# Performance work log

Hardware: AMD Instinct MI355X
Metric: run time of the kernel (lower is better)

The kernel has to match this reference:

```python
import jax, jax.numpy as jnp
import numpy as np

N_NODES = 100000
N_EDGES = 1600000
IN_F, HID_F, OUT_F = 128, 256, 64


def setup_inputs() -> dict:
    key = jax.random.key(0)
    ks = jax.random.split(key, 10)
    feats = jax.random.normal(ks[0], (N_NODES, IN_F), dtype=jnp.float32)
    edge_src = jax.random.randint(ks[1], (N_EDGES,), 0, N_NODES, dtype=jnp.int32)
    edge_dst = jax.random.randint(ks[2], (N_EDGES,), 0, N_NODES, dtype=jnp.int32)

    def glorot(k, shape):
        fan_in, fan_out = shape[1], shape[0]
        lim = np.sqrt(6.0 / (fan_in + fan_out)).astype(np.float32)
        return jax.random.uniform(k, shape, jnp.float32, -lim, lim)

    # layer 0: in -> hid, layer 1: hid -> hid, layer 2: hid -> out
    W0_self = glorot(ks[3], (HID_F, IN_F))
    W0_neigh = glorot(ks[4], (HID_F, IN_F))
    b0 = jnp.zeros((HID_F,), jnp.float32)
    W1_self = glorot(ks[5], (HID_F, HID_F))
    W1_neigh = glorot(ks[6], (HID_F, HID_F))
    b1 = jnp.zeros((HID_F,), jnp.float32)
    W2_self = glorot(ks[7], (OUT_F, HID_F))
    W2_neigh = glorot(ks[8], (OUT_F, HID_F))
    b2 = jnp.zeros((OUT_F,), jnp.float32)
    return {
        "features": feats, "edge_src": edge_src, "edge_dst": edge_dst,
        "W0_self": W0_self, "W0_neigh": W0_neigh, "b0": b0,
        "W1_self": W1_self, "W1_neigh": W1_neigh, "b1": b1,
        "W2_self": W2_self, "W2_neigh": W2_neigh, "b2": b2,
    }


def _mean_aggregate(h, src, dst, n_nodes):
    # gather source features per edge, scatter-sum to destinations, divide by in-degree
    msgs = h[src]                                            # [E, d]
    agg = jax.ops.segment_sum(msgs, dst, num_segments=n_nodes)  # [N, d]
    deg = jax.ops.segment_sum(jnp.ones_like(dst, dtype=h.dtype), dst, num_segments=n_nodes)
    deg = jnp.maximum(deg, 1.0)
    return agg / deg[:, None]


def _sage_conv(h, src, dst, W_self, W_neigh, b, act):
    h_neigh = _mean_aggregate(h, src, dst, h.shape[0])
    out = h @ W_self.T + h_neigh @ W_neigh.T + b
    return act(out) if act is not None else out


def reference(features, edge_src, edge_dst,
              W0_self, W0_neigh, b0,
              W1_self, W1_neigh, b1,
              W2_self, W2_neigh, b2):
    h = _sage_conv(features, edge_src, edge_dst, W0_self, W0_neigh, b0, jax.nn.relu)
    h = _sage_conv(h, edge_src, edge_dst, W1_self, W1_neigh, b1, jax.nn.relu)
    h = _sage_conv(h, edge_src, edge_dst, W2_self, W2_neigh, b2, None)
    return h
```

## Files before the change

### kernel.cpp

```cpp
#include <hip/hip_runtime.h>


constexpr int NN = 100000;
constexpr int NE = 1600000;

typedef short s16x8 __attribute__((ext_vector_type(8)));
typedef float f32x4 __attribute__((ext_vector_type(4)));

struct ushort4_t { unsigned short x, y, z, w; };
struct ushort2_t { unsigned short x, y; };

__device__ __forceinline__ float bf2f(unsigned short u) {
    union { unsigned int i; float f; } c; c.i = ((unsigned int)u) << 16; return c.f;
}
__device__ __forceinline__ unsigned short f2bf(float f) {
    union { float f; unsigned int i; } c; c.f = f;
    unsigned int r = (c.i + 0x7fffu + ((c.i >> 16) & 1u)) >> 16;
    return (unsigned short)r;
}

__global__ void deg_hist_kernel(const int* __restrict__ dst, int* __restrict__ degi, int n) {
    int e = blockIdx.x * blockDim.x + threadIdx.x;
    if (e < n) atomicAdd(&degi[dst[e]], 1);
}

constexpr int SCHUNK = 1024;
constexpr int NCH = (NN + SCHUNK - 1) / SCHUNK;
constexpr int NB = (NN + 255) / 256;

__global__ void chunk_sum_kernel(const int* __restrict__ degi, int* __restrict__ csum) {
    __shared__ int red[256];
    const int blk = blockIdx.x, t = threadIdx.x;
    const int base = blk * SCHUNK + t * 4;
    int s = 0;
#pragma unroll
    for (int u = 0; u < 4; ++u) { const int i = base + u; if (i < NN) s += degi[i]; }
    red[t] = s;
    __syncthreads();
    for (int o = 128; o > 0; o >>= 1) {
        if (t < o) red[t] += red[t + o];
        __syncthreads();
    }
    if (t == 0) csum[blk] = red[0];
}

__global__ void chunk_scan_kernel(const int* __restrict__ csum, int* __restrict__ coff,
                                  int* __restrict__ row_start) {
    __shared__ int sh[128];
    const int t = threadIdx.x;
    const int v0 = (t < NCH) ? csum[t] : 0;
    sh[t] = v0;
    __syncthreads();
    for (int o = 1; o < 128; o <<= 1) {
        const int v = (t >= o) ? sh[t - o] : 0;
        __syncthreads();
        sh[t] += v;
        __syncthreads();
    }
    if (t < NCH) coff[t] = sh[t] - v0;
    if (t == 0) row_start[NN] = NE;
}

__global__ void scan_write_kernel(const int* __restrict__ degi, const int* __restrict__ coff,
                                  int* __restrict__ row_start, int* __restrict__ gcur,
                                  float* __restrict__ rdeg) {
    __shared__ int sh[256];
    const int blk = blockIdx.x, t = threadIdx.x;
    const int base = blk * SCHUNK + t * 4;
    int d[4]; int s = 0;
#pragma unroll
    for (int u = 0; u < 4; ++u) { const int i = base + u; d[u] = (i < NN) ? degi[i] : 0; s += d[u]; }
    sh[t] = s;
    __syncthreads();
    for (int o = 1; o < 256; o <<= 1) {
        const int v = (t >= o) ? sh[t - o] : 0;
        __syncthreads();
        sh[t] += v;
        __syncthreads();
    }
    int run = coff[blk] + sh[t] - s;
#pragma unroll
    for (int u = 0; u < 4; ++u) {
        const int i = base + u;
        if (i < NN) {
            row_start[i] = run;
            if ((i & 255) == 0) gcur[i >> 8] = run;
            rdeg[i] = 1.0f / (float)max(d[u], 1);
            run += d[u];
        }
    }
}

constexpr int EPB_A = 4096;
__global__ __launch_bounds__(256) void bucket_scatter_kernel(
    const int* __restrict__ src, const int* __restrict__ dst,
    int* __restrict__ gcur, int2* __restrict__ ebuf) {
    __shared__ int hist[NB];
    __shared__ int base[NB];
    const int blk = blockIdx.x, t = threadIdx.x;
    int myS[16], myD[16];
#pragma unroll
    for (int u = 0; u < 16; ++u) {
        const int i = blk * EPB_A + u * 256 + t;
        if (i < NE) { myS[u] = src[i]; myD[u] = dst[i]; } else myD[u] = -1;
    }
    for (int b = t; b < NB; b += 256) hist[b] = 0;
    __syncthreads();
#pragma unroll
    for (int u = 0; u < 16; ++u)
        if (myD[u] >= 0) atomicAdd(&hist[myD[u] >> 8], 1);
    __syncthreads();
    for (int b = t; b < NB; b += 256) {
        const int c = hist[b];
        base[b] = c ? atomicAdd(&gcur[b], c) : 0;
    }
    __syncthreads();
    for (int b = t; b < NB; b += 256) hist[b] = 0;
    __syncthreads();
#pragma unroll
    for (int u = 0; u < 16; ++u)
        if (myD[u] >= 0) {
            const int bk = myD[u] >> 8;
            const int off = atomicAdd(&hist[bk], 1);
            ebuf[base[bk] + off] = make_int2(myS[u], myD[u]);
        }
}

__global__ __launch_bounds__(256) void bucket_fill_kernel(
    const int2* __restrict__ ebuf, const int* __restrict__ row_start,
    int* __restrict__ csr) {
    __shared__ int lcur[256];
    const int b = blockIdx.x, t = threadIdx.x;
    const int nbase = b << 8;
    const int nend = min(nbase + 256, NN);
    if (nbase + t < nend) lcur[t] = row_start[nbase + t];
    __syncthreads();
    const int beg = row_start[nbase];
    const int end = row_start[nend];
    for (int i = beg + t; i < end; i += 256) {
        const int2 e = ebuf[i];
        const int p = atomicAdd(&lcur[e.y & 255], 1);
        csr[p] = e.x;
    }
}

__global__ void cvt_f32_bf16(const float* __restrict__ src, unsigned short* __restrict__ dst, int nquad) {
    int i = blockIdx.x * blockDim.x + threadIdx.x;
    if (i >= nquad) return;
    const float4 v = reinterpret_cast<const float4*>(src)[i];
    ushort4_t o = { f2bf(v.x), f2bf(v.y), f2bf(v.z), f2bf(v.w) };
    reinterpret_cast<ushort4_t*>(dst)[i] = o;
}

__global__ void cvt_weights(const float* a, const float* b, const float* c,
                            const float* d, const float* e, const float* f,
                            unsigned short* __restrict__ o) {
    int i = blockIdx.x * blockDim.x + threadIdx.x;
    int q = i * 4;
    if (q >= 229376) return;
    const float* s; int off;
    if      (q <  32768) { s = a; off = 0; }
    else if (q <  65536) { s = b; off = 32768; }
    else if (q < 131072) { s = c; off = 65536; }
    else if (q < 196608) { s = d; off = 131072; }
    else if (q < 212992) { s = e; off = 196608; }
    else                 { s = f; off = 212992; }
    const float4 v = *reinterpret_cast<const float4*>(s + (q - off));
    ushort4_t ov = { f2bf(v.x), f2bf(v.y), f2bf(v.z), f2bf(v.w) };
    *reinterpret_cast<ushort4_t*>(o + q) = ov;
}

template<int D>
__global__ __launch_bounds__(256) void gather_mean_bf16(
    const unsigned short* __restrict__ rows, const int* __restrict__ row_start,
    const int* __restrict__ csr, const float* __restrict__ rdeg,
    unsigned short* __restrict__ out) {
    constexpr int VPL = D / 64;
    const int node = (int)((blockIdx.x * (unsigned)blockDim.x + threadIdx.x) >> 6);
    if (node >= NN) return;
    const int lane = threadIdx.x & 63;
    const int beg = row_start[node];
    const int end = row_start[node + 1];
    float acc[VPL];
#pragma unroll
    for (int u = 0; u < VPL; ++u) acc[u] = 0.f;

    auto accum = [&](int s) {
        const unsigned short* p = rows + (size_t)s * D + lane * VPL;
        if constexpr (VPL == 4) {
            const ushort4_t v = *reinterpret_cast<const ushort4_t*>(p);
            acc[0] += bf2f(v.x); acc[1] += bf2f(v.y); acc[2] += bf2f(v.z); acc[3] += bf2f(v.w);
        } else if constexpr (VPL == 2) {
            const ushort2_t v = *reinterpret_cast<const ushort2_t*>(p);
            acc[0] += bf2f(v.x); acc[1] += bf2f(v.y);
        } else {
            acc[0] += bf2f(*p);
        }
    };

    int e = beg;
    for (; e + 8 <= end; e += 8) {
        const int s0 = csr[e],     s1 = csr[e + 1], s2 = csr[e + 2], s3 = csr[e + 3];
        const int s4 = csr[e + 4], s5 = csr[e + 5], s6 = csr[e + 6], s7 = csr[e + 7];
        accum(s0); accum(s1); accum(s2); accum(s3);
        accum(s4); accum(s5); accum(s6); accum(s7);
    }
    for (; e + 4 <= end; e += 4) {
        const int s0 = csr[e], s1 = csr[e + 1], s2 = csr[e + 2], s3 = csr[e + 3];
        accum(s0); accum(s1); accum(s2); accum(s3);
    }
    for (; e < end; ++e) accum(csr[e]);

    const float r = rdeg[node];
    unsigned short* o = out + (size_t)node * D + lane * VPL;
    if constexpr (VPL == 4) {
        ushort4_t v = { f2bf(acc[0] * r), f2bf(acc[1] * r), f2bf(acc[2] * r), f2bf(acc[3] * r) };
        *reinterpret_cast<ushort4_t*>(o) = v;
    } else if constexpr (VPL == 2) {
        ushort2_t v = { f2bf(acc[0] * r), f2bf(acc[1] * r) };
        *reinterpret_cast<ushort2_t*>(o) = v;
    } else {
        *o = f2bf(acc[0] * r);
    }
}

template<int K1, int K2, int F, int BN, bool RELU, bool HASBIAS, bool HASADD, bool OUTBF16>
__global__ __launch_bounds__(256, 2) void mfma_gemm(
    const unsigned short* A1, const unsigned short* A2,
    const unsigned short* __restrict__ W1, const unsigned short* __restrict__ W2,
    const float* __restrict__ bias, const unsigned short* __restrict__ addC,
    void* outp) {

    constexpr int BM = 128, BK = 64;
    constexpr int KA = K1 + K2;
    constexpr int WN = BN / 2;
    constexpr int FM = 4, FN = WN / 16;
    constexpr int ABASE = 0;
    constexpr int BBASE = BM * BK * 2;
    constexpr int B_ITERS = (BN * 8) / 256;

    __shared__ __align__(16) char smem[(BM + BN) * BK * 2];

    const int tid = threadIdx.x;
    const int l = tid & 63;
    const int w = tid >> 6;
    const int wr = w >> 1, wc = w & 1;
    const int lr = l & 15, lhi = l >> 4;
    const int bm = blockIdx.x * BM;
    const int bn = blockIdx.y * BN;

    f32x4 acc[FM][FN];
#pragma unroll
    for (int i = 0; i < FM; ++i)
#pragma unroll
        for (int j = 0; j < FN; ++j) acc[i][j] = (f32x4){0.f, 0.f, 0.f, 0.f};

    int rowA[FM], rowB[FN];
#pragma unroll
    for (int fm = 0; fm < FM; ++fm) rowA[fm] = wr * 64 + fm * 16 + lr;
#pragma unroll
    for (int fn = 0; fn < FN; ++fn) rowB[fn] = wc * WN + fn * 16 + lr;

    for (int k0 = 0; k0 < KA; k0 += BK) {
        const bool inR1 = (k0 < K1);
        const unsigned short* Ap = inR1 ? A1 : A2;
        const unsigned short* Wp = inR1 ? W1 : W2;
        const int stride = inR1 ? K1 : K2;
        const int kk0 = inR1 ? k0 : (k0 - K1);

#pragma unroll
        for (int it = 0; it < 4; ++it) {
            const int s = tid + it * 256;
            const int m = s >> 3;
            const int kseg = s & 7;
            float4 v = make_float4(0.f, 0.f, 0.f, 0.f);
            const int mg = bm + m;
            if (mg < NN)
                v = *reinterpret_cast<const float4*>(Ap + (size_t)mg * stride + kk0 + kseg * 8);
            *reinterpret_cast<float4*>(smem + ABASE + m * 128 + ((kseg ^ (m & 7)) << 4)) = v;
        }
#pragma unroll
        for (int it = 0; it < B_ITERS; ++it) {
            const int s = tid + it * 256;
            const int f = s >> 3;
            const int kseg = s & 7;
            const float4 v = *reinterpret_cast<const float4*>(
                Wp + (size_t)(bn + f) * stride + kk0 + kseg * 8);
            *reinterpret_cast<float4*>(smem + BBASE + f * 128 + ((kseg ^ (f & 7)) << 4)) = v;
        }
        __syncthreads();

#pragma unroll
        for (int ksub = 0; ksub < 2; ++ksub) {
            const int kb = ksub * 4 + lhi;
            s16x8 a[FM], b[FN];
#pragma unroll
            for (int fm = 0; fm < FM; ++fm)
                a[fm] = *reinterpret_cast<const s16x8*>(
                    smem + ABASE + rowA[fm] * 128 + ((kb ^ (rowA[fm] & 7)) << 4));
#pragma unroll
            for (int fn = 0; fn < FN; ++fn)
                b[fn] = *reinterpret_cast<const s16x8*>(
                    smem + BBASE + rowB[fn] * 128 + ((kb ^ (rowB[fn] & 7)) << 4));
#pragma unroll
            for (int fm = 0; fm < FM; ++fm)
#pragma unroll
                for (int fn = 0; fn < FN; ++fn)
                    acc[fm][fn] = __builtin_amdgcn_mfma_f32_16x16x32_bf16(
                        a[fm], b[fn], acc[fm][fn], 0, 0, 0);
        }
        __syncthreads();
    }

#pragma unroll
    for (int fn = 0; fn < FN; ++fn) {
        const int col = bn + wc * WN + fn * 16 + lr;
        const float bv = HASBIAS ? bias[col] : 0.f;
#pragma unroll
        for (int fm = 0; fm < FM; ++fm) {
#pragma unroll
            for (int r = 0; r < 4; ++r) {
                const int row = bm + wr * 64 + fm * 16 + lhi * 4 + r;
                if (row >= NN) continue;
                float v = acc[fm][fn][r] + bv;
                if (HASADD) v += bf2f(addC[(size_t)row * F + col]);
                if (RELU) v = fmaxf(v, 0.f);
                if (OUTBF16)
                    ((unsigned short*)outp)[(size_t)row * F + col] = f2bf(v);
                else
                    ((float*)outp)[(size_t)row * F + col] = v;
            }
        }
    }
}

extern "C" void kernel_launch(void* const* d_in, const int* in_sizes, int n_in,
                              void* d_out, int out_size, void* d_ws, size_t ws_size,
                              hipStream_t stream) {
    const float* feats = (const float*)d_in[0];
    const int*   esrc  = (const int*)d_in[1];
    const int*   edst  = (const int*)d_in[2];
    const float* W0s = (const float*)d_in[3];
    const float* W0n = (const float*)d_in[4];
    const float* b0  = (const float*)d_in[5];
    const float* W1s = (const float*)d_in[6];
    const float* W1n = (const float*)d_in[7];
    const float* b1  = (const float*)d_in[8];
    const float* W2s = (const float*)d_in[9];
    const float* W2n = (const float*)d_in[10];
    const float* b2  = (const float*)d_in[11];
    float* out = (float*)d_out;

    char* p = (char*)d_ws;
    auto alloc = [&](size_t bytes) { char* r = p; p += (bytes + 255) & ~255ull; return r; };
    int*   degi      = (int*)alloc((size_t)NN * 4);
    int*   row_start = (int*)alloc(((size_t)NN + 1) * 4);
    int*   gcur      = (int*)alloc((size_t)NB * 4);
    int*   csr       = (int*)alloc((size_t)NE * 4);
    int2*  ebuf      = (int2*)alloc((size_t)NE * 8);
    float* rdeg      = (float*)alloc((size_t)NN * 4);
    int*   csum      = (int*)alloc((size_t)NCH * 4);
    int*   coff      = (int*)alloc((size_t)NCH * 4);
    unsigned short* wbuf = (unsigned short*)alloc((size_t)229376 * 2);
    unsigned short* fx   = (unsigned short*)alloc((size_t)NN * 128 * 2);
    unsigned short* agg  = (unsigned short*)alloc((size_t)NN * 256 * 2);
    unsigned short* h1   = (unsigned short*)alloc((size_t)NN * 256 * 2);
    unsigned short* h2   = (unsigned short*)alloc((size_t)NN * 256 * 2);
    unsigned short* z    = agg;
    unsigned short* aggz = agg + (size_t)NN * 64;

    const unsigned short* w0s = wbuf;
    const unsigned short* w0n = wbuf + 32768;
    const unsigned short* w1s = wbuf + 65536;
    const unsigned short* w1n = wbuf + 131072;
    const unsigned short* w2s = wbuf + 196608;
    const unsigned short* w2n = wbuf + 212992;

    hipMemsetAsync(degi, 0, (size_t)NN * 4, stream);
    deg_hist_kernel<<<(NE + 255) / 256, 256, 0, stream>>>(edst, degi, NE);
    chunk_sum_kernel<<<NCH, 256, 0, stream>>>(degi, csum);
    chunk_scan_kernel<<<1, 128, 0, stream>>>(csum, coff, row_start);
    scan_write_kernel<<<NCH, 256, 0, stream>>>(degi, coff, row_start, gcur, rdeg);
    bucket_scatter_kernel<<<(NE + EPB_A - 1) / EPB_A, 256, 0, stream>>>(esrc, edst, gcur, ebuf);
    bucket_fill_kernel<<<NB, 256, 0, stream>>>(ebuf, row_start, csr);

    cvt_f32_bf16<<<(NN * 128 / 4 + 255) / 256, 256, 0, stream>>>(feats, fx, NN * 128 / 4);
    cvt_weights<<<(229376 / 4 + 255) / 256, 256, 0, stream>>>(W0s, W0n, W1s, W1n, W2s, W2n, wbuf);

    const int gather_grid = (NN + 3) / 4;
    const dim3 g256((NN + 127) / 128, 2);
    const dim3 g64((NN + 127) / 128, 1);

    gather_mean_bf16<128><<<gather_grid, 256, 0, stream>>>(fx, row_start, csr, rdeg, agg);
    mfma_gemm<128, 128, 256, 128, true, true, false, true>
        <<<g256, 256, 0, stream>>>(fx, agg, w0s, w0n, b0, nullptr, h1);

    gather_mean_bf16<256><<<gather_grid, 256, 0, stream>>>(h1, row_start, csr, rdeg, agg);
    mfma_gemm<256, 256, 256, 128, true, true, false, true>
        <<<g256, 256, 0, stream>>>(h1, agg, w1s, w1n, b1, nullptr, h2);

    mfma_gemm<256, 0, 64, 64, false, false, false, true>
        <<<g64, 256, 0, stream>>>(h2, nullptr, w2n, nullptr, nullptr, nullptr, z);
    gather_mean_bf16<64><<<gather_grid, 256, 0, stream>>>(z, row_start, csr, rdeg, aggz);
    mfma_gemm<256, 0, 64, 64, false, true, true, false>
        <<<g64, 256, 0, stream>>>(h2, nullptr, w2s, nullptr, b2, aggz, out);
}
```

Baseline: 619.0 us.

## Double-buffer GEMM shared-memory tiles using direct global-to-LDS loads

Replaces the register-staged global-to-LDS copy in the MFMA GEMM with `global_load_lds` 16-byte transfers that write straight into shared memory. The XOR swizzle now moves to the global address side. It also adds a two-stage ping-pong buffer, so the next K tile is fetched while MFMAs run on the current one, and drops one barrier per iteration. Out-of-range rows are clamped to row 0 instead of zero-filled. The cost is double the shared memory per block, which may lower occupancy for wider tiles.

```diff
diff --git a/kernel.cpp b/kernel.cpp
--- a/kernel.cpp
+++ b/kernel.cpp
@@ -17,6 +17,12 @@
     union { float f; unsigned int i; } c; c.f = f;
     unsigned int r = (c.i + 0x7fffu + ((c.i >> 16) & 1u)) >> 16;
     return (unsigned short)r;
+}
+
+__device__ __forceinline__ void gl16(const void* g, void* l) {
+    __builtin_amdgcn_global_load_lds(
+        (const __attribute__((address_space(1))) unsigned int*)g,
+        (__attribute__((address_space(3))) unsigned int*)l, 16, 0, 0);
 }
 
 __global__ void deg_hist_kernel(const int* __restrict__ dst, int* __restrict__ degi, int n) {
@@ -235,11 +241,11 @@
     constexpr int KA = K1 + K2;
     constexpr int WN = BN / 2;
     constexpr int FM = 4, FN = WN / 16;
-    constexpr int ABASE = 0;
     constexpr int BBASE = BM * BK * 2;
+    constexpr int BUFSZ = (BM + BN) * BK * 2;
     constexpr int B_ITERS = (BN * 8) / 256;
 
-    __shared__ __align__(16) char smem[(BM + BN) * BK * 2];
+    __shared__ __align__(16) char smem[2][BUFSZ];
 
     const int tid = threadIdx.x;
     const int l = tid & 63;
@@ -261,35 +267,37 @@
 #pragma unroll
     for (int fn = 0; fn < FN; ++fn) rowB[fn] = wc * WN + fn * 16 + lr;
 
-    for (int k0 = 0; k0 < KA; k0 += BK) {
+    auto stage = [&](int buf, int k0) {
         const bool inR1 = (k0 < K1);
         const unsigned short* Ap = inR1 ? A1 : A2;
         const unsigned short* Wp = inR1 ? W1 : W2;
         const int stride = inR1 ? K1 : K2;
         const int kk0 = inR1 ? k0 : (k0 - K1);
-
+        char* sb = smem[buf];
 #pragma unroll
         for (int it = 0; it < 4; ++it) {
             const int s = tid + it * 256;
-            const int m = s >> 3;
-            const int kseg = s & 7;
-            float4 v = make_float4(0.f, 0.f, 0.f, 0.f);
-            const int mg = bm + m;
-            if (mg < NN)
-                v = *reinterpret_cast<const float4*>(Ap + (size_t)mg * stride + kk0 + kseg * 8);
-            *reinterpret_cast<float4*>(smem + ABASE + m * 128 + ((kseg ^ (m & 7)) << 4)) = v;
+            const int m = s >> 3, kseg = s & 7;
+            int mg = bm + m;
+            if (mg >= NN) mg = 0;
+            gl16(Ap + (size_t)mg * stride + kk0 + ((kseg ^ (m & 7)) << 3), sb + s * 16);
         }
 #pragma unroll
         for (int it = 0; it < B_ITERS; ++it) {
             const int s = tid + it * 256;
-            const int f = s >> 3;
-            const int kseg = s & 7;
-            const float4 v = *reinterpret_cast<const float4*>(
-                Wp + (size_t)(bn + f) * stride + kk0 + kseg * 8);
-            *reinterpret_cast<float4*>(smem + BBASE + f * 128 + ((kseg ^ (f & 7)) << 4)) = v;
-        }
-        __syncthreads();
-
+            const int f = s >> 3, kseg = s & 7;
+            gl16(Wp + (size_t)(bn + f) * stride + kk0 + ((kseg ^ (f & 7)) << 3),
+                 sb + BBASE + s * 16);
+        }
+    };
+
+    stage(0, 0);
+    __syncthreads();
+
+    int cur = 0;
+    for (int k0 = 0; k0 < KA; k0 += BK) {
+        if (k0 + BK < KA) stage(cur ^ 1, k0 + BK);
+        const char* sb = smem[cur];
 #pragma unroll
         for (int ksub = 0; ksub < 2; ++ksub) {
             const int kb = ksub * 4 + lhi;
@@ -297,11 +305,11 @@
 #pragma unroll
             for (int fm = 0; fm < FM; ++fm)
                 a[fm] = *reinterpret_cast<const s16x8*>(
-                    smem + ABASE + rowA[fm] * 128 + ((kb ^ (rowA[fm] & 7)) << 4));
+                    sb + rowA[fm] * 128 + ((kb ^ (rowA[fm] & 7)) << 4));
 #pragma unroll
             for (int fn = 0; fn < FN; ++fn)
                 b[fn] = *reinterpret_cast<const s16x8*>(
-                    smem + BBASE + rowB[fn] * 128 + ((kb ^ (rowB[fn] & 7)) << 4));
+                    sb + BBASE + rowB[fn] * 128 + ((kb ^ (rowB[fn] & 7)) << 4));
 #pragma unroll
             for (int fm = 0; fm < FM; ++fm)
 #pragma unroll
@@ -310,6 +318,7 @@
                         a[fm], b[fn], acc[fm][fn], 0, 0, 0);
         }
         __syncthreads();
+        cur ^= 1;
     }
 
 #pragma unroll
```

After: 629.6 us. No clear change (+1.7%).

## Build CSR via bucket counts and use sub-wavefront gathers with wider loads

Applied to the files above, without the earlier changes.

Replaces the per-node degree histogram, with its global atomics and three-kernel scan, by a block-local bucket count, a single-block bucket scan, and a bucket_build kernel. That kernel computes per-node degrees, row_start and rdeg in shared memory before filling the CSR. Separately, the gather kernels now assign sub-wavefront groups of 32 or 16 lanes per node with 16-byte loads, so more nodes are processed per wave and loads are wider. The build change removes a memset, several launches and 1.6M global atomics. The cost is an extra pass over ebuf and less lane-level parallelism per node.

```diff
diff --git a/kernel.cpp b/kernel.cpp
--- a/kernel.cpp
+++ b/kernel.cpp
@@ -5,10 +5,10 @@
 constexpr int NE = 1600000;
 
 typedef short s16x8 __attribute__((ext_vector_type(8)));
+typedef unsigned short u16x8 __attribute__((ext_vector_type(8)));
 typedef float f32x4 __attribute__((ext_vector_type(4)));
 
 struct ushort4_t { unsigned short x, y, z, w; };
-struct ushort2_t { unsigned short x, y; };
 
 __device__ __forceinline__ float bf2f(unsigned short u) {
     union { unsigned int i; float f; } c; c.i = ((unsigned int)u) << 16; return c.f;
@@ -19,79 +19,43 @@
     return (unsigned short)r;
 }
 
-__global__ void deg_hist_kernel(const int* __restrict__ dst, int* __restrict__ degi, int n) {
-    int e = blockIdx.x * blockDim.x + threadIdx.x;
-    if (e < n) atomicAdd(&degi[dst[e]], 1);
-}
-
-constexpr int SCHUNK = 1024;
-constexpr int NCH = (NN + SCHUNK - 1) / SCHUNK;
 constexpr int NB = (NN + 255) / 256;
-
-__global__ void chunk_sum_kernel(const int* __restrict__ degi, int* __restrict__ csum) {
-    __shared__ int red[256];
+constexpr int EPB_A = 4096;
+constexpr int NBLK_E = (NE + EPB_A - 1) / EPB_A;
+
+__global__ __launch_bounds__(256) void bucket_count_kernel(
+    const int* __restrict__ dst, int* __restrict__ bcnt) {
+    __shared__ int hist[NB];
     const int blk = blockIdx.x, t = threadIdx.x;
-    const int base = blk * SCHUNK + t * 4;
-    int s = 0;
-#pragma unroll
-    for (int u = 0; u < 4; ++u) { const int i = base + u; if (i < NN) s += degi[i]; }
-    red[t] = s;
-    __syncthreads();
-    for (int o = 128; o > 0; o >>= 1) {
-        if (t < o) red[t] += red[t + o];
-        __syncthreads();
-    }
-    if (t == 0) csum[blk] = red[0];
-}
-
-__global__ void chunk_scan_kernel(const int* __restrict__ csum, int* __restrict__ coff,
-                                  int* __restrict__ row_start) {
-    __shared__ int sh[128];
+    for (int b = t; b < NB; b += 256) hist[b] = 0;
+    __syncthreads();
+#pragma unroll
+    for (int u = 0; u < 16; ++u) {
+        const int i = blk * EPB_A + u * 256 + t;
+        if (i < NE) atomicAdd(&hist[dst[i] >> 8], 1);
+    }
+    __syncthreads();
+    for (int b = t; b < NB; b += 256)
+        if (hist[b]) atomicAdd(&bcnt[b], hist[b]);
+}
+
+__global__ void bucket_scan_kernel(const int* __restrict__ bcnt, int* __restrict__ bbase,
+                                   int* __restrict__ gcur, int* __restrict__ row_start) {
+    __shared__ int sh[512];
     const int t = threadIdx.x;
-    const int v0 = (t < NCH) ? csum[t] : 0;
+    const int v0 = (t < NB) ? bcnt[t] : 0;
     sh[t] = v0;
     __syncthreads();
-    for (int o = 1; o < 128; o <<= 1) {
+    for (int o = 1; o < 512; o <<= 1) {
         const int v = (t >= o) ? sh[t - o] : 0;
         __syncthreads();
         sh[t] += v;
         __syncthreads();
     }
-    if (t < NCH) coff[t] = sh[t] - v0;
-    if (t == 0) row_start[NN] = NE;
-}
-
-__global__ void scan_write_kernel(const int* __restrict__ degi, const int* __restrict__ coff,
-                                  int* __restrict__ row_start, int* __restrict__ gcur,
-                                  float* __restrict__ rdeg) {
-    __shared__ int sh[256];
-    const int blk = blockIdx.x, t = threadIdx.x;
-    const int base = blk * SCHUNK + t * 4;
-    int d[4]; int s = 0;
-#pragma unroll
-    for (int u = 0; u < 4; ++u) { const int i = base + u; d[u] = (i < NN) ? degi[i] : 0; s += d[u]; }
-    sh[t] = s;
-    __syncthreads();
-    for (int o = 1; o < 256; o <<= 1) {
-        const int v = (t >= o) ? sh[t - o] : 0;
-        __syncthreads();
-        sh[t] += v;
-        __syncthreads();
-    }
-    int run = coff[blk] + sh[t] - s;
-#pragma unroll
-    for (int u = 0; u < 4; ++u) {
-        const int i = base + u;
-        if (i < NN) {
-            row_start[i] = run;
-            if ((i & 255) == 0) gcur[i >> 8] = run;
-            rdeg[i] = 1.0f / (float)max(d[u], 1);
-            run += d[u];
-        }
-    }
-}
-
-constexpr int EPB_A = 4096;
+    if (t < NB) { const int e = sh[t] - v0; bbase[t] = e; gcur[t] = e; }
+    if (t == 0) { bbase[NB] = NE; row_start[NN] = NE; }
+}
+
 __global__ __launch_bounds__(256) void bucket_scatter_kernel(
     const int* __restrict__ src, const int* __restrict__ dst,
     int* __restrict__ gcur, int2* __restrict__ ebuf) {
@@ -126,17 +90,36 @@
         }
 }
 
-__global__ __launch_bounds__(256) void bucket_fill_kernel(
-    const int2* __restrict__ ebuf, const int* __restrict__ row_start,
-    int* __restrict__ csr) {
+__global__ __launch_bounds__(256) void bucket_build_kernel(
+    const int2* __restrict__ ebuf, const int* __restrict__ bbase,
+    int* __restrict__ row_start, float* __restrict__ rdeg, int* __restrict__ csr) {
+    __shared__ int deg[256];
+    __shared__ int sh[256];
     __shared__ int lcur[256];
     const int b = blockIdx.x, t = threadIdx.x;
-    const int nbase = b << 8;
-    const int nend = min(nbase + 256, NN);
-    if (nbase + t < nend) lcur[t] = row_start[nbase + t];
-    __syncthreads();
-    const int beg = row_start[nbase];
-    const int end = row_start[nend];
+    const int beg = bbase[b], end = bbase[b + 1];
+    deg[t] = 0;
+    __syncthreads();
+    for (int i = beg + t; i < end; i += 256)
+        atomicAdd(&deg[ebuf[i].y & 255], 1);
+    __syncthreads();
+    const int d = deg[t];
+    sh[t] = d;
+    __syncthreads();
+    for (int o = 1; o < 256; o <<= 1) {
+        const int v = (t >= o) ? sh[t - o] : 0;
+        __syncthreads();
+        sh[t] += v;
+        __syncthreads();
+    }
+    const int node = (b << 8) + t;
+    const int rs = beg + sh[t] - d;
+    if (node < NN) {
+        row_start[node] = rs;
+        rdeg[node] = 1.0f / (float)max(d, 1);
+    }
+    lcur[t] = rs;
+    __syncthreads();
     for (int i = beg + t; i < end; i += 256) {
         const int2 e = ebuf[i];
         const int p = atomicAdd(&lcur[e.y & 255], 1);
@@ -170,31 +153,34 @@
     *reinterpret_cast<ushort4_t*>(o + q) = ov;
 }
 
-template<int D>
+template<int D, int SUBW>
 __global__ __launch_bounds__(256) void gather_mean_bf16(
     const unsigned short* __restrict__ rows, const int* __restrict__ row_start,
     const int* __restrict__ csr, const float* __restrict__ rdeg,
     unsigned short* __restrict__ out) {
-    constexpr int VPL = D / 64;
-    const int node = (int)((blockIdx.x * (unsigned)blockDim.x + threadIdx.x) >> 6);
+    constexpr int BPL = 2 * D / SUBW;
+    constexpr int EPL = BPL / 2;
+    constexpr int NPB = 256 / SUBW;
+    const int sg   = threadIdx.x / SUBW;
+    const int lane = threadIdx.x % SUBW;
+    const int node = blockIdx.x * NPB + sg;
     if (node >= NN) return;
-    const int lane = threadIdx.x & 63;
     const int beg = row_start[node];
     const int end = row_start[node + 1];
-    float acc[VPL];
-#pragma unroll
-    for (int u = 0; u < VPL; ++u) acc[u] = 0.f;
+
+    float acc[EPL];
+#pragma unroll
+    for (int u = 0; u < EPL; ++u) acc[u] = 0.f;
 
     auto accum = [&](int s) {
-        const unsigned short* p = rows + (size_t)s * D + lane * VPL;
-        if constexpr (VPL == 4) {
+        const unsigned short* p = rows + (size_t)s * D + lane * EPL;
+        if constexpr (BPL == 16) {
+            const u16x8 v = *reinterpret_cast<const u16x8*>(p);
+#pragma unroll
+            for (int u = 0; u < 8; ++u) acc[u] += bf2f((unsigned short)v[u]);
+        } else {
             const ushort4_t v = *reinterpret_cast<const ushort4_t*>(p);
             acc[0] += bf2f(v.x); acc[1] += bf2f(v.y); acc[2] += bf2f(v.z); acc[3] += bf2f(v.w);
-        } else if constexpr (VPL == 2) {
-            const ushort2_t v = *reinterpret_cast<const ushort2_t*>(p);
-            acc[0] += bf2f(v.x); acc[1] += bf2f(v.y);
-        } else {
-            acc[0] += bf2f(*p);
         }
     };
 
@@ -205,22 +191,18 @@
         accum(s0); accum(s1); accum(s2); accum(s3);
         accum(s4); accum(s5); accum(s6); accum(s7);
     }
-    for (; e + 4 <= end; e += 4) {
-        const int s0 = csr[e], s1 = csr[e + 1], s2 = csr[e + 2], s3 = csr[e + 3];
-        accum(s0); accum(s1); accum(s2); accum(s3);
-    }
     for (; e < end; ++e) accum(csr[e]);
 
     const float r = rdeg[node];
-    unsigned short* o = out + (size_t)node * D + lane * VPL;
-    if constexpr (VPL == 4) {
+    unsigned short* o = out + (size_t)node * D + lane * EPL;
+    if constexpr (BPL == 16) {
+        u16x8 v;
+#pragma unroll
+        for (int u = 0; u < 8; ++u) v[u] = (unsigned short)f2bf(acc[u] * r);
+        *reinterpret_cast<u16x8*>(o) = v;
+    } else {
         ushort4_t v = { f2bf(acc[0] * r), f2bf(acc[1] * r), f2bf(acc[2] * r), f2bf(acc[3] * r) };
         *reinterpret_cast<ushort4_t*>(o) = v;
-    } else if constexpr (VPL == 2) {
-        ushort2_t v = { f2bf(acc[0] * r), f2bf(acc[1] * r) };
-        *reinterpret_cast<ushort2_t*>(o) = v;
-    } else {
-        *o = f2bf(acc[0] * r);
     }
 }
 
@@ -353,14 +335,13 @@
 
     char* p = (char*)d_ws;
     auto alloc = [&](size_t bytes) { char* r = p; p += (bytes + 255) & ~255ull; return r; };
-    int*   degi      = (int*)alloc((size_t)NN * 4);
     int*   row_start = (int*)alloc(((size_t)NN + 1) * 4);
+    int*   bcnt      = (int*)alloc((size_t)NB * 4);
+    int*   bbase     = (int*)alloc(((size_t)NB + 1) * 4);
     int*   gcur      = (int*)alloc((size_t)NB * 4);
     int*   csr       = (int*)alloc((size_t)NE * 4);
     int2*  ebuf      = (int2*)alloc((size_t)NE * 8);
     float* rdeg      = (float*)alloc((size_t)NN * 4);
-    int*   csum      = (int*)alloc((size_t)NCH * 4);
-    int*   coff      = (int*)alloc((size_t)NCH * 4);
     unsigned short* wbuf = (unsigned short*)alloc((size_t)229376 * 2);
     unsigned short* fx   = (unsigned short*)alloc((size_t)NN * 128 * 2);
     unsigned short* agg  = (unsigned short*)alloc((size_t)NN * 256 * 2);
@@ -376,32 +357,29 @@
     const unsigned short* w2s = wbuf + 196608;
     const unsigned short* w2n = wbuf + 212992;
 
-    hipMemsetAsync(degi, 0, (size_t)NN * 4, stream);
-    deg_hist_kernel<<<(NE + 255) / 256, 256, 0, stream>>>(edst, degi, NE);
-    chunk_sum_kernel<<<NCH, 256, 0, stream>>>(degi, csum);
-    chunk_scan_kernel<<<1, 128, 0, stream>>>(csum, coff, row_start);
-    scan_write_kernel<<<NCH, 256, 0, stream>>>(degi, coff, row_start, gcur, rdeg);
-    bucket_scatter_kernel<<<(NE + EPB_A - 1) / EPB_A, 256, 0, stream>>>(esrc, edst, gcur, ebuf);
-    bucket_fill_kernel<<<NB, 256, 0, stream>>>(ebuf, row_start, csr);
+    hipMemsetAsync(bcnt, 0, (size_t)NB * 4, stream);
+    bucket_count_kernel<<<NBLK_E, 256, 0, stream>>>(edst, bcnt);
+    bucket_scan_kernel<<<1, 512, 0, stream>>>(bcnt, bbase, gcur, row_start);
+    bucket_scatter_kernel<<<NBLK_E, 256, 0, stream>>>(esrc, edst, gcur, ebuf);
+    bucket_build_kernel<<<NB, 256, 0, stream>>>(ebuf, bbase, row_start, rdeg, csr);
 
     cvt_f32_bf16<<<(NN * 128 / 4 + 255) / 256, 256, 0, stream>>>(feats, fx, NN * 128 / 4);
     cvt_weights<<<(229376 / 4 + 255) / 256, 256, 0, stream>>>(W0s, W0n, W1s, W1n, W2s, W2n, wbuf);
 
-    const int gather_grid = (NN + 3) / 4;
     const dim3 g256((NN + 127) / 128, 2);
     const dim3 g64((NN + 127) / 128, 1);
 
-    gather_mean_bf16<128><<<gather_grid, 256, 0, stream>>>(fx, row_start, csr, rdeg, agg);
+    gather_mean_bf16<128, 32><<<(NN + 7) / 8, 256, 0, stream>>>(fx, row_start, csr, rdeg, agg);
     mfma_gemm<128, 128, 256, 128, true, true, false, true>
         <<<g256, 256, 0, stream>>>(fx, agg, w0s, w0n, b0, nullptr, h1);
 
-    gather_mean_bf16<256><<<gather_grid, 256, 0, stream>>>(h1, row_start, csr, rdeg, agg);
+    gather_mean_bf16<256, 32><<<(NN + 7) / 8, 256, 0, stream>>>(h1, row_start, csr, rdeg, agg);
     mfma_gemm<256, 256, 256, 128, true, true, false, true>
         <<<g256, 256, 0, stream>>>(h1, agg, w1s, w1n, b1, nullptr, h2);
 
     mfma_gemm<256, 0, 64, 64, false, false, false, true>
         <<<g64, 256, 0, stream>>>(h2, nullptr, w2n, nullptr, nullptr, nullptr, z);
-    gather_mean_bf16<64><<<gather_grid, 256, 0, stream>>>(z, row_start, csr, rdeg, aggz);
+    gather_mean_bf16<64, 16><<<(NN + 15) / 16, 256, 0, stream>>>(z, row_start, csr, rdeg, aggz);
     mfma_gemm<256, 0, 64, 64, false, true, true, false>
         <<<g64, 256, 0, stream>>>(h2, nullptr, w2s, nullptr, b2, aggz, out);
 }
```

Result: faster. 554.7 us (-10.4%).
